# Performance work log

Hardware: AMD Instinct MI355X
Metric: run time of the kernel (lower is better)

The kernel has to match this reference:

```python
import jax, jax.numpy as jnp
import numpy as np

DIM = 768
HEADS = 12
HEAD_DIM = DIM // HEADS          # 64
DIM_HALF = HEAD_DIM // 2         # 32
SPATIAL = 3


def _rope_cos_sin(grid, voxel_size, theta):
    """grid: static tuple of ints (len SPATIAL); voxel_size: [SPATIAL] float;
    theta: [H, DIM_HALF] per-head frequency spectrum.
    Returns cos, sin of shape [H, N, DIM_HALF] where N = prod(grid)."""
    axes = [jnp.arange(g, dtype=theta.dtype) for g in grid]
    mesh = jnp.meshgrid(*axes, indexing='ij')
    coords = jnp.stack([m.reshape(-1) for m in mesh], axis=-1) * voxel_size  # [N, S] physical coords
    axis_idx = np.arange(DIM_HALF) % len(grid)        # round-robin freq->axis assignment
    pos = coords[:, axis_idx]                          # [N, DIM_HALF]
    ang = pos[None, :, :] * theta[:, None, :]          # [H, N, DIM_HALF]
    return jnp.cos(ang), jnp.sin(ang)


def _rope_apply(t, cos, sin):
    # t: [B, H, N, D]; cos/sin: [H, N, DIM_HALF] broadcast over batch
    t1, t2 = jnp.split(t, 2, axis=-1)
    return jnp.concatenate([t1 * cos - t2 * sin, t1 * sin + t2 * cos], axis=-1)


def setup_inputs() -> dict:
    key = jax.random.key(0)
    k_x, k_qkv, k_proj, k_b = jax.random.split(key, 4)
    B, N = 2, 8 * 16 * 16
    x = jax.random.normal(k_x, (B, N, DIM), dtype=jnp.float32)
    voxel_size = jnp.ones((SPATIAL,), dtype=jnp.float32)
    # nn.Linear weights are [out_features, in_features]
    w_qkv = jax.random.normal(k_qkv, (3 * DIM, DIM), dtype=jnp.float32) * (DIM ** -0.5)
    w_proj = jax.random.normal(k_proj, (DIM, DIM), dtype=jnp.float32) * (DIM ** -0.5)
    b_proj = jax.random.normal(k_b, (DIM,), dtype=jnp.float32) * 0.02
    # learnable per-head base frequencies: theta_j = 10000^{-j/dim_half}
    base = (1.0 / (10000.0 ** (np.arange(DIM_HALF, dtype=np.float32) / DIM_HALF)))
    theta = jnp.asarray(np.tile(base[None, :], (HEADS, 1)))  # [H, DIM_HALF]
    return {"x": x, "voxel_size": voxel_size, "w_qkv": w_qkv, "w_proj": w_proj,
            "b_proj": b_proj, "theta": theta, "grid_d": 8, "grid_h": 16, "grid_w": 16}


def reference(x, voxel_size, w_qkv, w_proj, b_proj, theta, grid_d, grid_h, grid_w):
    B, N, dim = x.shape
    H, D = HEADS, HEAD_DIM
    qkv = jnp.einsum('bnd,ed->bne', x, w_qkv).reshape(B, N, 3, H, D)
    qkv = jnp.transpose(qkv, (2, 0, 3, 1, 4))           # [3, B, H, N, D]
    q, k, v = qkv[0], qkv[1], qkv[2]
    cos, sin = _rope_cos_sin((grid_d, grid_h, grid_w), voxel_size, theta)
    q = _rope_apply(q, cos, sin)
    k = _rope_apply(k, cos, sin)
    scale = 1.0 / np.sqrt(D).astype(np.float32)
    attn = jax.nn.softmax(jnp.einsum('bhnd,bhmd->bhnm', q, k) * scale, axis=-1)
    out = jnp.einsum('bhnm,bhmd->bhnd', attn, v)        # [B, H, N, D]
    out = jnp.transpose(out, (0, 2, 1, 3)).reshape(B, N, dim)
    return out @ w_proj.T + b_proj
```

## Files before the change

### kernel.cpp

```cpp
#include <hip/hip_runtime.h>
#include <stdint.h>

#define DIM 768
#define NHEADS 12
#define HDIM 64
#define DHALF 32
#define NTOK 2048
#define LOG2E 1.44269504088896340736f

typedef unsigned short u16;
typedef unsigned int u32;
typedef __bf16 bf16x8 __attribute__((ext_vector_type(8)));
typedef short s16x8 __attribute__((ext_vector_type(8)));
typedef float f32x4 __attribute__((ext_vector_type(4)));

__device__ __forceinline__ f32x4 f4zero() { f32x4 z = {0.f, 0.f, 0.f, 0.f}; return z; }

__device__ __forceinline__ u16 f2bf(float f) {
    u32 u = __builtin_bit_cast(u32, f);
    u32 r = (u + 0x7FFFu + ((u >> 16) & 1u)) >> 16;
    return (u16)r;
}

__device__ __forceinline__ void gld_lds16(void* lds, const void* g) {
    __builtin_amdgcn_global_load_lds((const __attribute__((address_space(1))) u32*)g,
                                     (__attribute__((address_space(3))) u32*)lds,
                                     16, 0, 0);
}

__global__ __launch_bounds__(256) void cast3_f32_to_bf16(const float* __restrict__ a, u16* __restrict__ oa, int na4,
                                                         const float* __restrict__ b, u16* __restrict__ ob, int nb4,
                                                         const float* __restrict__ c, u16* __restrict__ oc, int nc4) {
    int i = blockIdx.x * 256 + threadIdx.x;
    const float* src;
    u16* dst;
    int j = i;
    if (i < na4) { src = a; dst = oa; }
    else if (i < na4 + nb4) { src = b; dst = ob; j = i - na4; }
    else if (i < na4 + nb4 + nc4) { src = c; dst = oc; j = i - na4 - nb4; }
    else return;
    float4 v = ((const float4*)src)[j];
    u32 w0 = (u32)f2bf(v.x) | ((u32)f2bf(v.y) << 16);
    u32 w1 = (u32)f2bf(v.z) | ((u32)f2bf(v.w) << 16);
    ((uint2*)dst)[j] = make_uint2(w0, w1);
}

__global__ __launch_bounds__(256) void gemm_bt(const u16* __restrict__ A, const u16* __restrict__ Bm,
                                               float* __restrict__ C, const float* __restrict__ bias,
                                               int M, int N, int K) {
    __shared__ __align__(16) u16 sA[2][128 * 32];
    __shared__ __align__(16) u16 sB[2][128 * 32];
    const int t = threadIdx.x;
    const int wave = t >> 6, lane = t & 63;
    const int quad = lane >> 4, l16 = lane & 15;
    const int bm = blockIdx.y * 128, bn = blockIdx.x * 128;
    const int wr = wave >> 1, wc = wave & 1;

    f32x4 acc[4][4];
#pragma unroll
    for (int i = 0; i < 4; i++)
#pragma unroll
        for (int j = 0; j < 4; j++) acc[i][j] = f4zero();

    auto stage = [&](int k0, int bi) {
#pragma unroll
        for (int r = 0; r < 2; ++r) {
            int c = (r * 4 + wave) * 64 + lane;
            int row = c >> 2, kc = c & 3;
            gld_lds16((char*)&sA[bi][0] + (size_t)(r * 4 + wave) * 1024,
                      A + (size_t)(bm + row) * K + k0 + kc * 8);
            gld_lds16((char*)&sB[bi][0] + (size_t)(r * 4 + wave) * 1024,
                      Bm + (size_t)(bn + row) * K + k0 + kc * 8);
        }
    };

    stage(0, 0);
    int cur = 0;
    for (int k0 = 0; k0 < K; k0 += 32) {
        __syncthreads();
        if (k0 + 32 < K) stage(k0 + 32, cur ^ 1);
        const u16* pA = &sA[cur][0];
        const u16* pB = &sB[cur][0];
        bf16x8 af[4], bfr[4];
#pragma unroll
        for (int mb = 0; mb < 4; mb++)
            af[mb] = *(const bf16x8*)(pA + (wr * 64 + mb * 16 + l16) * 32 + quad * 8);
#pragma unroll
        for (int nb = 0; nb < 4; nb++)
            bfr[nb] = *(const bf16x8*)(pB + (wc * 64 + nb * 16 + l16) * 32 + quad * 8);
#pragma unroll
        for (int mb = 0; mb < 4; mb++)
#pragma unroll
            for (int nb = 0; nb < 4; nb++)
                acc[mb][nb] = __builtin_amdgcn_mfma_f32_16x16x32_bf16(af[mb], bfr[nb], acc[mb][nb], 0, 0, 0);
        cur ^= 1;
    }
#pragma unroll
    for (int mb = 0; mb < 4; mb++)
#pragma unroll
        for (int nb = 0; nb < 4; nb++) {
            int col = bn + wc * 64 + nb * 16 + l16;
            float bv = bias ? bias[col] : 0.f;
#pragma unroll
            for (int r = 0; r < 4; r++) {
                int row = bm + wr * 64 + mb * 16 + quad * 4 + r;
                C[(size_t)row * N + col] = acc[mb][nb][r] + bv;
            }
        }
}

__global__ __launch_bounds__(256) void prep(const float* __restrict__ qkv,
                                            const float* __restrict__ voxel,
                                            const float* __restrict__ theta,
                                            const int* __restrict__ gh_p, const int* __restrict__ gw_p,
                                            u16* __restrict__ q_s, u16* __restrict__ k_s,
                                            u16* __restrict__ vT, int B, int nrope) {
    __shared__ u16 tile[64][66];
    int bid = blockIdx.x;
    int t = threadIdx.x;
    if (bid < nrope) {
        int tid = bid * 256 + t;
        int d = tid & (DHALF - 1);
        int n = (tid >> 5) & (NTOK - 1);
        int hb = tid >> 16;
        int h = hb % NHEADS;
        int b = hb / NHEADS;
        int gh = *gh_p, gw = *gw_p;
        int xw = n % gw;
        int rem = n / gw;
        int yh = rem % gh;
        int zd = rem / gh;
        int axis = d % 3;
        float coordv = (axis == 0 ? (float)zd : (axis == 1 ? (float)yh : (float)xw)) * voxel[axis];
        float ang = coordv * theta[h * DHALF + d];
        float s, c;
        __sincosf(ang, &s, &c);
        size_t bi = ((size_t)b * NTOK + n) * (3 * DIM);
        const float* qp = qkv + bi + h * HDIM;
        float q1 = qp[d], q2 = qp[d + DHALF];
        float k1 = qp[DIM + d], k2 = qp[DIM + d + DHALF];
        size_t bh = (size_t)b * NHEADS + h;
        size_t bo = (bh * NTOK + n) * HDIM;
        const float qscale = 0.125f * LOG2E;
        q_s[bo + d] = f2bf((q1 * c - q2 * s) * qscale);
        q_s[bo + d + DHALF] = f2bf((q1 * s + q2 * c) * qscale);
        int tile_i = n >> 6, r = n & 63, g = r >> 4, k16 = r & 15;
        int qd = d >> 3, j = d & 7;
        size_t off = bh * NTOK * HDIM + (size_t)tile_i * 4096 +
                     (size_t)(g * 2) * 512 + (qd * 16 + k16) * 8 + j;
        k_s[off] = f2bf(k1 * c - k2 * s);
        k_s[off + 512] = f2bf(k1 * s + k2 * c);
    } else {
        int idx = bid - nrope;
        int nt = idx & 31;
        int rem = idx >> 5;
        int h = rem % NHEADS, b = rem / NHEADS;
        int n_loc = t >> 2, d0 = (t & 3) * 16;
        const float* src = qkv + ((size_t)b * NTOK + nt * 64 + n_loc) * (3 * DIM) + 2 * DIM + h * HDIM + d0;
#pragma unroll
        for (int j = 0; j < 16; j += 4) {
            float4 v = *(const float4*)(src + j);
            tile[n_loc][d0 + j + 0] = f2bf(v.x);
            tile[n_loc][d0 + j + 1] = f2bf(v.y);
            tile[n_loc][d0 + j + 2] = f2bf(v.z);
            tile[n_loc][d0 + j + 3] = f2bf(v.w);
        }
        __syncthreads();
        int db = t >> 6, l = t & 63, q = (t >> 4) & 3, l16 = t & 15;
        int dd = db * 16 + l16;
        size_t bh = (size_t)b * NHEADS + h;
#pragma unroll
        for (int c = 0; c < 2; c++) {
            u32 w[4];
#pragma unroll
            for (int jp = 0; jp < 4; jp++) {
                int jj0 = jp * 2, jj1 = jp * 2 + 1;
                int key0 = c * 32 + (jj0 < 4 ? 4 * q + jj0 : 16 + 4 * q + jj0 - 4);
                int key1 = c * 32 + (jj1 < 4 ? 4 * q + jj1 : 16 + 4 * q + jj1 - 4);
                w[jp] = (u32)tile[key0][dd] | ((u32)tile[key1][dd] << 16);
            }
            u16* dst = vT + ((bh * 64 + (size_t)nt * 2 + c) * 2048 + db * 512 + (size_t)l * 8);
            *(uint4*)dst = make_uint4(w[0], w[1], w[2], w[3]);
        }
    }
}

__global__ __launch_bounds__(256) void flash_attn(const u16* __restrict__ Q, const u16* __restrict__ Kp,
                                                  const u16* __restrict__ Vp, u16* __restrict__ Out, int NBH) {
    int i = blockIdx.x;
    int bh_i = i % NBH;
    int qt = i / NBH;
    int b = bh_i / NHEADS, h = bh_i % NHEADS;
    int t = threadIdx.x, wave = t >> 6, lane = t & 63, quad = lane >> 4, l16 = lane & 15;
    size_t bh = (size_t)b * NHEADS + h;
    const u16* Qb = Q + bh * NTOK * HDIM;
    const u16* Kb = Kp + bh * NTOK * HDIM;
    const u16* Vb = Vp + bh * NTOK * HDIM;

    __shared__ __align__(16) u16 smem[2][8192];

    const int q0 = qt * 64 + wave * 16;
    bf16x8 qf[2];
#pragma unroll
    for (int kc = 0; kc < 2; kc++)
        qf[kc] = *(const bf16x8*)(Qb + (size_t)(q0 + l16) * HDIM + kc * 32 + quad * 8);

    s16x8 ov;
#pragma unroll
    for (int j = 0; j < 8; j++) ov[j] = (l16 == 0) ? (short)0x3F80 : (short)0;

    f32x4 o[5];
#pragma unroll
    for (int db = 0; db < 5; db++) o[db] = f4zero();

    auto stage = [&](int kt, int bi) {
        const u16* Kg = Kb + (size_t)kt * 4096;
        const u16* Vg = Vb + (size_t)kt * 4096;
        u16* buf = &smem[bi][0];
#pragma unroll
        for (int s = 0; s < 2; s++) {
            gld_lds16(buf + (wave * 2 + s) * 512, Kg + (wave * 2 + s) * 512 + lane * 8);
            gld_lds16(buf + 4096 + (wave * 2 + s) * 512, Vg + (wave * 2 + s) * 512 + lane * 8);
        }
    };

    stage(0, 0);
    int cur = 0;
    for (int kt = 0; kt < NTOK / 64; ++kt) {
        __syncthreads();
        if (kt + 1 < NTOK / 64) stage(kt + 1, cur ^ 1);
        const u16* sK = &smem[cur][0];
        const u16* sV = &smem[cur][4096];
#pragma unroll
        for (int c = 0; c < 2; ++c) {
            bf16x8 kf[2][2];
#pragma unroll
            for (int kb2 = 0; kb2 < 2; kb2++)
#pragma unroll
                for (int kc = 0; kc < 2; kc++)
                    kf[kb2][kc] = *(const bf16x8*)(sK + ((c * 2 + kb2) * 2 + kc) * 512 + lane * 8);
            s16x8 bv[4];
#pragma unroll
            for (int db = 0; db < 4; db++)
                bv[db] = *(const s16x8*)(sV + c * 2048 + db * 512 + lane * 8);
            f32x4 st0, st1;
            {
                f32x4 z = f4zero();
                z = __builtin_amdgcn_mfma_f32_16x16x32_bf16(kf[0][0], qf[0], z, 0, 0, 0);
                st0 = __builtin_amdgcn_mfma_f32_16x16x32_bf16(kf[0][1], qf[1], z, 0, 0, 0);
                f32x4 z2 = f4zero();
                z2 = __builtin_amdgcn_mfma_f32_16x16x32_bf16(kf[1][0], qf[0], z2, 0, 0, 0);
                st1 = __builtin_amdgcn_mfma_f32_16x16x32_bf16(kf[1][1], qf[1], z2, 0, 0, 0);
            }
            bf16x8 pb;
#pragma unroll
            for (int r = 0; r < 4; r++) {
                pb[r] = (__bf16)__builtin_exp2f(st0[r]);
                pb[r + 4] = (__bf16)__builtin_exp2f(st1[r]);
            }
#pragma unroll
            for (int db = 0; db < 4; db++)
                o[db] = __builtin_amdgcn_mfma_f32_16x16x32_bf16(pb, __builtin_bit_cast(bf16x8, bv[db]),
                                                                o[db], 0, 0, 0);
            o[4] = __builtin_amdgcn_mfma_f32_16x16x32_bf16(pb, __builtin_bit_cast(bf16x8, ov),
                                                           o[4], 0, 0, 0);
        }
        cur ^= 1;
    }

#pragma unroll
    for (int r = 0; r < 4; r++) {
        float s = __shfl(o[4][r], lane & 48);
        float inv = 1.0f / s;
        int n = q0 + quad * 4 + r;
        u16* dst = Out + ((size_t)b * NTOK + n) * DIM + h * HDIM + l16;
#pragma unroll
        for (int db = 0; db < 4; db++)
            dst[db * 16] = f2bf(o[db][r] * inv);
    }
}

extern "C" void kernel_launch(void* const* d_in, const int* in_sizes, int n_in,
                              void* d_out, int out_size, void* d_ws, size_t ws_size,
                              hipStream_t stream) {
    const float* x = (const float*)d_in[0];
    const float* voxel = (const float*)d_in[1];
    const float* w_qkv = (const float*)d_in[2];
    const float* w_proj = (const float*)d_in[3];
    const float* b_proj = (const float*)d_in[4];
    const float* theta = (const float*)d_in[5];
    const int* gh_p = (const int*)d_in[7];
    const int* gw_p = (const int*)d_in[8];
    const int B = in_sizes[0] / (NTOK * DIM);
    const int M = B * NTOK;

    char* p = (char*)d_ws;
    u16* xb = (u16*)p;       p += (size_t)M * DIM * 2;
    u16* wqkvb = (u16*)p;    p += (size_t)3 * DIM * DIM * 2;
    u16* wprojb = (u16*)p;   p += (size_t)DIM * DIM * 2;
    float* qkv = (float*)p;  p += (size_t)M * 3 * DIM * 4;
    u16* q_s = (u16*)p;      p += (size_t)M * DIM * 2;
    u16* k_s = (u16*)p;      p += (size_t)M * DIM * 2;
    u16* vT = (u16*)p;       p += (size_t)M * DIM * 2;
    u16* attn = (u16*)p;     p += (size_t)M * DIM * 2;

    int na4 = M * DIM / 4, nb4 = 3 * DIM * DIM / 4, nc4 = DIM * DIM / 4;
    cast3_f32_to_bf16<<<dim3((na4 + nb4 + nc4 + 255) / 256), 256, 0, stream>>>(
        x, xb, na4, w_qkv, wqkvb, nb4, w_proj, wprojb, nc4);

    gemm_bt<<<dim3(3 * DIM / 128, M / 128), 256, 0, stream>>>(xb, wqkvb, qkv, nullptr, M, 3 * DIM, DIM);

    int nrope = (B * NHEADS * NTOK * DHALF) / 256;
    int nvt = B * NHEADS * (NTOK / 64);
    prep<<<dim3(nrope + nvt), 256, 0, stream>>>(qkv, voxel, theta, gh_p, gw_p, q_s, k_s, vT, B, nrope);

    flash_attn<<<dim3((B * NHEADS * NTOK) / 64), 256, 0, stream>>>(q_s, k_s, vT, attn, B * NHEADS);

    gemm_bt<<<dim3(DIM / 128, M / 128), 256, 0, stream>>>(attn, wprojb, (float*)d_out, b_proj, M, DIM, DIM);
}
```

Measured before the change: 190.5 us.

## Fuse RoPE and Q/K/V layout packing into the QKV GEMM epilogue

```diff
diff --git a/kernel.cpp b/kernel.cpp
--- a/kernel.cpp
+++ b/kernel.cpp
@@ -6,6 +6,7 @@
 #define HDIM 64
 #define DHALF 32
 #define NTOK 2048
+#define QKVN 2304
 #define LOG2E 1.44269504088896340736f
 
 typedef unsigned short u16;
@@ -109,79 +110,125 @@
         }
 }
 
-__global__ __launch_bounds__(256) void prep(const float* __restrict__ qkv,
-                                            const float* __restrict__ voxel,
-                                            const float* __restrict__ theta,
-                                            const int* __restrict__ gh_p, const int* __restrict__ gw_p,
-                                            u16* __restrict__ q_s, u16* __restrict__ k_s,
-                                            u16* __restrict__ vT, int B, int nrope) {
-    __shared__ u16 tile[64][66];
-    int bid = blockIdx.x;
-    int t = threadIdx.x;
-    if (bid < nrope) {
-        int tid = bid * 256 + t;
-        int d = tid & (DHALF - 1);
-        int n = (tid >> 5) & (NTOK - 1);
-        int hb = tid >> 16;
-        int h = hb % NHEADS;
-        int b = hb / NHEADS;
-        int gh = *gh_p, gw = *gw_p;
-        int xw = n % gw;
-        int rem = n / gw;
-        int yh = rem % gh;
-        int zd = rem / gh;
-        int axis = d % 3;
-        float coordv = (axis == 0 ? (float)zd : (axis == 1 ? (float)yh : (float)xw)) * voxel[axis];
-        float ang = coordv * theta[h * DHALF + d];
-        float s, c;
-        __sincosf(ang, &s, &c);
-        size_t bi = ((size_t)b * NTOK + n) * (3 * DIM);
-        const float* qp = qkv + bi + h * HDIM;
-        float q1 = qp[d], q2 = qp[d + DHALF];
-        float k1 = qp[DIM + d], k2 = qp[DIM + d + DHALF];
-        size_t bh = (size_t)b * NHEADS + h;
-        size_t bo = (bh * NTOK + n) * HDIM;
-        const float qscale = 0.125f * LOG2E;
-        q_s[bo + d] = f2bf((q1 * c - q2 * s) * qscale);
-        q_s[bo + d + DHALF] = f2bf((q1 * s + q2 * c) * qscale);
-        int tile_i = n >> 6, r = n & 63, g = r >> 4, k16 = r & 15;
-        int qd = d >> 3, j = d & 7;
-        size_t off = bh * NTOK * HDIM + (size_t)tile_i * 4096 +
-                     (size_t)(g * 2) * 512 + (qd * 16 + k16) * 8 + j;
-        k_s[off] = f2bf(k1 * c - k2 * s);
-        k_s[off + 512] = f2bf(k1 * s + k2 * c);
+__global__ __launch_bounds__(256) void gemm_qkv_rope(const u16* __restrict__ A, const u16* __restrict__ Bm,
+                                                     const float* __restrict__ voxel,
+                                                     const float* __restrict__ theta,
+                                                     const int* __restrict__ gh_p, const int* __restrict__ gw_p,
+                                                     u16* __restrict__ q_s, u16* __restrict__ k_s,
+                                                     u16* __restrict__ vT, int M) {
+    __shared__ __align__(16) u16 sA[2][128 * 32];
+    __shared__ __align__(16) u16 sB[2][128 * 32];
+    const int t = threadIdx.x;
+    const int wave = t >> 6, lane = t & 63;
+    const int quad = lane >> 4, l16 = lane & 15;
+    const int bm = blockIdx.y * 128, bn = blockIdx.x * 128;
+    const int wr = wave >> 1, wc = wave & 1;
+    const int K = DIM;
+
+    f32x4 acc[4][4];
+#pragma unroll
+    for (int i = 0; i < 4; i++)
+#pragma unroll
+        for (int j = 0; j < 4; j++) acc[i][j] = f4zero();
+
+    auto stage = [&](int k0, int bi) {
+#pragma unroll
+        for (int r = 0; r < 2; ++r) {
+            int c = (r * 4 + wave) * 64 + lane;
+            int row = c >> 2, kc = c & 3;
+            gld_lds16((char*)&sA[bi][0] + (size_t)(r * 4 + wave) * 1024,
+                      A + (size_t)(bm + row) * K + k0 + kc * 8);
+            gld_lds16((char*)&sB[bi][0] + (size_t)(r * 4 + wave) * 1024,
+                      Bm + (size_t)(bn + row) * K + k0 + kc * 8);
+        }
+    };
+
+    stage(0, 0);
+    int cur = 0;
+    for (int k0 = 0; k0 < K; k0 += 32) {
+        __syncthreads();
+        if (k0 + 32 < K) stage(k0 + 32, cur ^ 1);
+        const u16* pA = &sA[cur][0];
+        const u16* pB = &sB[cur][0];
+        bf16x8 af[4], bfr[4];
+#pragma unroll
+        for (int mb = 0; mb < 4; mb++)
+            af[mb] = *(const bf16x8*)(pA + (wr * 64 + mb * 16 + l16) * 32 + quad * 8);
+#pragma unroll
+        for (int nb = 0; nb < 4; nb++)
+            bfr[nb] = *(const bf16x8*)(pB + (wc * 64 + nb * 16 + l16) * 32 + quad * 8);
+#pragma unroll
+        for (int mb = 0; mb < 4; mb++)
+#pragma unroll
+            for (int nb = 0; nb < 4; nb++)
+                acc[mb][nb] = __builtin_amdgcn_mfma_f32_16x16x32_bf16(af[mb], bfr[nb], acc[mb][nb], 0, 0, 0);
+        cur ^= 1;
+    }
+
+    const int col0 = bn + wc * 64;
+    const int typ = col0 / DIM;
+    const int h = (col0 % DIM) >> 6;
+    const int b = bm / NTOK;
+    const int n0 = (bm % NTOK) + wr * 64;
+    const size_t bh = (size_t)b * NHEADS + h;
+
+    if (typ == 2) {
+        int nt = n0 >> 6;
+        u16* base = vT + (bh * 64 + (size_t)nt * 2) * 2048;
+#pragma unroll
+        for (int c2 = 0; c2 < 2; c2++)
+#pragma unroll
+            for (int nb = 0; nb < 4; nb++) {
+                u32 w0 = (u32)f2bf(acc[2 * c2][nb][0]) | ((u32)f2bf(acc[2 * c2][nb][1]) << 16);
+                u32 w1 = (u32)f2bf(acc[2 * c2][nb][2]) | ((u32)f2bf(acc[2 * c2][nb][3]) << 16);
+                u32 w2 = (u32)f2bf(acc[2 * c2 + 1][nb][0]) | ((u32)f2bf(acc[2 * c2 + 1][nb][1]) << 16);
+                u32 w3 = (u32)f2bf(acc[2 * c2 + 1][nb][2]) | ((u32)f2bf(acc[2 * c2 + 1][nb][3]) << 16);
+                *(uint4*)(base + (size_t)c2 * 2048 + nb * 512 + lane * 8) = make_uint4(w0, w1, w2, w3);
+            }
     } else {
-        int idx = bid - nrope;
-        int nt = idx & 31;
-        int rem = idx >> 5;
-        int h = rem % NHEADS, b = rem / NHEADS;
-        int n_loc = t >> 2, d0 = (t & 3) * 16;
-        const float* src = qkv + ((size_t)b * NTOK + nt * 64 + n_loc) * (3 * DIM) + 2 * DIM + h * HDIM + d0;
-#pragma unroll
-        for (int j = 0; j < 16; j += 4) {
-            float4 v = *(const float4*)(src + j);
-            tile[n_loc][d0 + j + 0] = f2bf(v.x);
-            tile[n_loc][d0 + j + 1] = f2bf(v.y);
-            tile[n_loc][d0 + j + 2] = f2bf(v.z);
-            tile[n_loc][d0 + j + 3] = f2bf(v.w);
-        }
-        __syncthreads();
-        int db = t >> 6, l = t & 63, q = (t >> 4) & 3, l16 = t & 15;
-        int dd = db * 16 + l16;
-        size_t bh = (size_t)b * NHEADS + h;
-#pragma unroll
-        for (int c = 0; c < 2; c++) {
-            u32 w[4];
-#pragma unroll
-            for (int jp = 0; jp < 4; jp++) {
-                int jj0 = jp * 2, jj1 = jp * 2 + 1;
-                int key0 = c * 32 + (jj0 < 4 ? 4 * q + jj0 : 16 + 4 * q + jj0 - 4);
-                int key1 = c * 32 + (jj1 < 4 ? 4 * q + jj1 : 16 + 4 * q + jj1 - 4);
-                w[jp] = (u32)tile[key0][dd] | ((u32)tile[key1][dd] << 16);
-            }
-            u16* dst = vT + ((bh * 64 + (size_t)nt * 2 + c) * 2048 + db * 512 + (size_t)l * 8);
-            *(uint4*)dst = make_uint4(w[0], w[1], w[2], w[3]);
-        }
+        const int gh = *gh_p, gw = *gw_p;
+        const float qsc = (typ == 0) ? 0.125f * LOG2E : 1.0f;
+        const float th0 = theta[h * DHALF + l16];
+        const float th1 = theta[h * DHALF + 16 + l16];
+        const int ax0 = l16 % 3, ax1 = (16 + l16) % 3;
+        const float vx0 = voxel[ax0], vx1 = voxel[ax1];
+#pragma unroll
+        for (int mb = 0; mb < 4; mb++)
+#pragma unroll
+            for (int r = 0; r < 4; r++) {
+                int n = n0 + mb * 16 + quad * 4 + r;
+                int xw = n % gw;
+                int rem = n / gw;
+                int yh = rem % gh;
+                int zd = rem / gh;
+                float c0 = (float)(ax0 == 0 ? zd : (ax0 == 1 ? yh : xw)) * vx0;
+                float c1 = (float)(ax1 == 0 ? zd : (ax1 == 1 ? yh : xw)) * vx1;
+                float s0, co0, s1, co1;
+                __sincosf(c0 * th0, &s0, &co0);
+                __sincosf(c1 * th1, &s1, &co1);
+                float t1a = acc[mb][0][r], t2a = acc[mb][2][r];
+                float o1a = (t1a * co0 - t2a * s0) * qsc, o2a = (t1a * s0 + t2a * co0) * qsc;
+                float t1b = acc[mb][1][r], t2b = acc[mb][3][r];
+                float o1b = (t1b * co1 - t2b * s1) * qsc, o2b = (t1b * s1 + t2b * co1) * qsc;
+                if (typ == 0) {
+                    u16* dq = q_s + (bh * NTOK + n) * HDIM;
+                    dq[l16] = f2bf(o1a);
+                    dq[l16 + DHALF] = f2bf(o2a);
+                    dq[16 + l16] = f2bf(o1b);
+                    dq[48 + l16] = f2bf(o2b);
+                } else {
+                    int tile_i = n >> 6;
+                    int k16 = quad * 4 + r;
+                    size_t baseo = bh * (size_t)NTOK * HDIM + (size_t)tile_i * 4096 + mb * 1024;
+                    int j = l16 & 7;
+                    size_t oa = baseo + (size_t)(((l16 >> 3) * 16 + k16) * 8 + j);
+                    size_t ob = baseo + (size_t)((((2 + (l16 >> 3)) * 16) + k16) * 8 + j);
+                    k_s[oa] = f2bf(o1a);
+                    k_s[oa + 512] = f2bf(o2a);
+                    k_s[ob] = f2bf(o1b);
+                    k_s[ob + 512] = f2bf(o2b);
+                }
+            }
     }
 }
 
@@ -298,7 +345,6 @@
     u16* xb = (u16*)p;       p += (size_t)M * DIM * 2;
     u16* wqkvb = (u16*)p;    p += (size_t)3 * DIM * DIM * 2;
     u16* wprojb = (u16*)p;   p += (size_t)DIM * DIM * 2;
-    float* qkv = (float*)p;  p += (size_t)M * 3 * DIM * 4;
     u16* q_s = (u16*)p;      p += (size_t)M * DIM * 2;
     u16* k_s = (u16*)p;      p += (size_t)M * DIM * 2;
     u16* vT = (u16*)p;       p += (size_t)M * DIM * 2;
@@ -308,11 +354,8 @@
     cast3_f32_to_bf16<<<dim3((na4 + nb4 + nc4 + 255) / 256), 256, 0, stream>>>(
         x, xb, na4, w_qkv, wqkvb, nb4, w_proj, wprojb, nc4);
 
-    gemm_bt<<<dim3(3 * DIM / 128, M / 128), 256, 0, stream>>>(xb, wqkvb, qkv, nullptr, M, 3 * DIM, DIM);
-
-    int nrope = (B * NHEADS * NTOK * DHALF) / 256;
-    int nvt = B * NHEADS * (NTOK / 64);
-    prep<<<dim3(nrope + nvt), 256, 0, stream>>>(qkv, voxel, theta, gh_p, gw_p, q_s, k_s, vT, B, nrope);
+    gemm_qkv_rope<<<dim3(QKVN / 128, M / 128), 256, 0, stream>>>(
+        xb, wqkvb, voxel, theta, gh_p, gw_p, q_s, k_s, vT, M);
 
     flash_attn<<<dim3((B * NHEADS * NTOK) / 64), 256, 0, stream>>>(q_s, k_s, vT, attn, B * NHEADS);
 
```

Result: faster. 180.4 us (-5.3%).
